# Optimization experiments

Hardware: AMD Instinct MI355X
Metric: run time of the kernel (lower is better)

The kernel has to match this reference:

```python
import jax, jax.numpy as jnp
import numpy as np

D = 1024        # number of Hawkes dimensions (N_g * K)
M = 32768       # number of events
BETA = 1.0      # fixed exponential-kernel decay
T_MAX = 1000    # observation horizon
EPS_MU = 1e-06
EPS_LOG = 1e-08


def setup_inputs() -> dict:
    key = jax.random.key(0)
    k1, k2, k3, k4 = jax.random.split(key, 4)
    t_events = jnp.sort(jax.random.uniform(k1, (M,), dtype=jnp.float32) * T_MAX)
    marks = jax.random.randint(k2, (M,), 0, D)
    # learned params around the torch init (-3 / -4) with a little noise
    log_mu = jnp.full((D,), -3.0, dtype=jnp.float32) + 0.1 * jax.random.normal(k3, (D,), dtype=jnp.float32)
    log_alpha = jnp.full((D, D), -4.0, dtype=jnp.float32) + 0.1 * jax.random.normal(k4, (D, D), dtype=jnp.float32)
    return {"t_events": t_events, "marks": marks, "log_mu": log_mu,
            "log_alpha": log_alpha, "T_max": T_MAX}


def reference(t_events, marks, log_mu, log_alpha, T_max):
    """Hawkes log-likelihood; faithful translation of XuHawkesTorch.intensity_loglik."""
    mu = jax.nn.softplus(log_mu) + EPS_MU          # [D]
    alpha = jax.nn.softplus(log_alpha)             # [D, D]
    T_max = jnp.asarray(T_max, dtype=t_events.dtype)

    # inter-event gaps; dt[0] = 0 so first event sees no decay (matches torch loop)
    dt = jnp.diff(t_events, prepend=t_events[:1])  # [M]
    decay = jnp.exp(-BETA * dt)                    # [M]

    def step(S, inp):
        dec, d = inp
        S = dec * S                                # exp-decay of excitation state
        lam_d = mu[d] + alpha[d] @ S               # intensity at event d
        ll = jnp.log(lam_d + EPS_LOG)
        S = S.at[d].add(1.0)                       # event adds unit excitation
        return S, ll

    S0 = jnp.zeros((D,), dtype=t_events.dtype)
    _, lls = jax.lax.scan(step, S0, (decay, marks))

    # compensator integral over [0, T_max]
    one_minus_exp = 1.0 - jnp.exp(-BETA * (T_max - t_events))   # [M]
    contrib = jax.ops.segment_sum(one_minus_exp, marks, num_segments=D)  # [D]
    integral = mu * T_max + alpha @ (contrib / BETA)            # [D]

    return lls.sum() - integral.sum()
```

## Files before the change

kernel.cpp:

```cpp
#include <hip/hip_runtime.h>


#define D 1024
#define M 32768
#define C 64
#define NC (M / C)
#define NB (NC * 4)
#define NG 16
#define GC (NC / NG)
#define TMAXV 1000.0f
#define EPSMU 1e-6f
#define EPSLOG 1e-8f

__device__ __forceinline__ float softplus(float x) {
    return (x > 0.0f) ? (x + log1pf(__expf(-x))) : log1pf(__expf(x));
}

__device__ __forceinline__ unsigned short f2bf(float x) {
    unsigned u = __float_as_uint(x);
    return (unsigned short)((u + 0x7FFFu + ((u >> 16) & 1u)) >> 16);
}
__device__ __forceinline__ float bf2f(unsigned short h) {
    return __uint_as_float(((unsigned)h) << 16);
}

__global__ void k_prep(const float* __restrict__ log_alpha, const float* __restrict__ log_mu,
                       unsigned short* __restrict__ ab, float* __restrict__ mu,
                       float* __restrict__ P) {
    int t = threadIdx.x;
    int b = blockIdx.x;
    if (b < 256) {
        int r0 = b * 4;
        float4 cs = {0.f, 0.f, 0.f, 0.f};
        for (int r = 0; r < 4; ++r) {
            const float4* src = (const float4*)(log_alpha + (size_t)(r0 + r) * D);
            float4 v = src[t];
            float4 a;
            a.x = softplus(v.x);
            a.y = softplus(v.y);
            a.z = softplus(v.z);
            a.w = softplus(v.w);
            cs.x += a.x; cs.y += a.y; cs.z += a.z; cs.w += a.w;
            ushort4 h;
            h.x = f2bf(a.x); h.y = f2bf(a.y); h.z = f2bf(a.z); h.w = f2bf(a.w);
            ((ushort4*)(ab + (size_t)(r0 + r) * D))[t] = h;
        }
        ((float4*)(P + (size_t)b * D))[t] = cs;
    } else {
#pragma unroll
        for (int q = 0; q < 4; ++q) {
            int k = t + 256 * q;
            mu[k] = softplus(log_mu[k]) + EPSMU;
        }
    }
}

__global__ void k_colred(const float* __restrict__ P, float* __restrict__ colsum) {
    __shared__ float red[8][32];
    int t = threadIdx.x;
    int colL = t & 31, seg = t >> 5;
    int col = blockIdx.x * 32 + colL;
    float s = 0.0f;
#pragma unroll 8
    for (int j = 0; j < 32; ++j)
        s += P[(size_t)(seg * 32 + j) * D + col];
    red[seg][colL] = s;
    __syncthreads();
    if (t < 32) {
        float v = 0.0f;
#pragma unroll
        for (int k = 0; k < 8; ++k) v += red[k][t];
        colsum[blockIdx.x * 32 + t] = v;
    }
}

__global__ void k_fused(const float* __restrict__ t_ev, const int* __restrict__ marks,
                        float* __restrict__ Sl, float* __restrict__ A) {
    __shared__ float Lh[GC * 256];
    __shared__ float dec[GC];
    __shared__ float tns[GC];
    int g = blockIdx.x >> 2, db = blockIdx.x & 3;
    int t = threadIdx.x;
#pragma unroll
    for (int q = 0; q < GC; ++q) Lh[q * 256 + t] = 0.0f;
    if (t < GC) {
        int gc = g * GC + t;
        float tn = (gc + 1 < NC) ? t_ev[(gc + 1) * C] : t_ev[M - 1];
        tns[t] = tn;
        dec[t] = (gc + 1 < NC) ? __expf(t_ev[gc * C] - tn) : 1.0f;
    }
    __syncthreads();
    int base = g * (GC * C);
#pragma unroll
    for (int it = 0; it < 8; ++it) {
        int e = it * 256 + t;
        float te = t_ev[base + e];
        int m = marks[base + e];
        int lc = e >> 6;
        int ml = m - db * 256;
        if ((unsigned)ml < 256u) atomicAdd(&Lh[lc * 256 + ml], __expf(te - tns[lc]));
    }
    __syncthreads();
    int k = db * 256 + t;
    float S = 0.0f;
    for (int lc = 0; lc < GC; ++lc) {
        Sl[(size_t)(g * GC + lc) * D + k] = S;
        S = S * dec[lc] + Lh[lc * 256 + t];
    }
    A[(size_t)g * D + k] = S;
}

__global__ void k_scanB(const float* __restrict__ t_ev, const float* __restrict__ A,
                        float* __restrict__ Sg, float* __restrict__ cumdec) {
    __shared__ float dec[NC];
    __shared__ float P[NG];
    int t = threadIdx.x;
    if (t < NC)
        dec[t] = (t + 1 < NC) ? __expf(t_ev[t * C] - t_ev[(t + 1) * C]) : 1.0f;
    __syncthreads();
    if (t < NC) {
        int g = t >> 5, r = t & 31;
        float p = 1.0f;
        for (int j = 0; j < r; ++j) p *= dec[g * GC + j];
        cumdec[t] = p;
        if (r == GC - 1) P[g] = p * dec[t];
    }
    __syncthreads();
    float a[NG];
#pragma unroll
    for (int g2 = 0; g2 < NG; ++g2) a[g2] = A[(size_t)g2 * D + t];
    float S = 0.0f;
#pragma unroll
    for (int g2 = 0; g2 < NG; ++g2) {
        Sg[(size_t)g2 * D + t] = S;
        S = S * P[g2] + a[g2];
    }
}

__launch_bounds__(256)
__global__ void k_main(const float* __restrict__ t_ev, const int* __restrict__ marks,
                       const unsigned short* __restrict__ ab, const float* __restrict__ mu,
                       const float* __restrict__ colsum, const float* __restrict__ Sl,
                       const float* __restrict__ Sg, const float* __restrict__ cumdec,
                       float* __restrict__ llp, float* __restrict__ compp) {
    __shared__ float S_lds[D];
    __shared__ float t_lds[C];
    __shared__ int d_lds[C];
    __shared__ float red[8];
    int t = threadIdx.x;
    int c = blockIdx.x >> 2, sub = blockIdx.x & 3;
    int g = c >> 5;
    float cd = cumdec[c];
#pragma unroll
    for (int q = 0; q < 4; ++q) {
        int k = t + 256 * q;
        S_lds[k] = Sl[(size_t)c * D + k] + Sg[(size_t)g * D + k] * cd;
    }
    if (t < C) {
        t_lds[t] = t_ev[c * C + t];
        d_lds[t] = marks[c * C + t];
    }
    __syncthreads();
    int wave = t >> 6, lane = t & 63;
    float t0 = t_lds[0];
    float ll_acc = 0.0f, comp_acc = 0.0f;
    for (int i = sub * 16 + wave; i < sub * 16 + 16; i += 4) {
        int row = d_lds[i];
        float ti = t_lds[i];
        float mu_r = mu[row];
        float cs_r = colsum[row];
        const uint4* arow = (const uint4*)(ab + (size_t)row * D);
        float acc_dot = 0.0f;
#pragma unroll
        for (int u = 0; u < 2; ++u) {
            uint4 pk = arow[2 * lane + u];
            const float4* sp = (const float4*)(S_lds + 16 * lane + 8 * u);
            float4 s0 = sp[0], s1 = sp[1];
            acc_dot += __uint_as_float(pk.x << 16) * s0.x
                     + __uint_as_float(pk.x & 0xFFFF0000u) * s0.y
                     + __uint_as_float(pk.y << 16) * s0.z
                     + __uint_as_float(pk.y & 0xFFFF0000u) * s0.w
                     + __uint_as_float(pk.z << 16) * s1.x
                     + __uint_as_float(pk.z & 0xFFFF0000u) * s1.y
                     + __uint_as_float(pk.w << 16) * s1.z
                     + __uint_as_float(pk.w & 0xFFFF0000u) * s1.w;
        }
        float part = acc_dot * __expf(t0 - ti);
        if (lane < i) {
            part += bf2f(ab[(size_t)row * D + d_lds[lane]]) * __expf(t_lds[lane] - ti);
        }
#pragma unroll
        for (int off = 32; off > 0; off >>= 1) part += __shfl_xor(part, off);
        if (lane == 0) {
            ll_acc += __logf(mu_r + part + EPSLOG);
            comp_acc += cs_r * (1.0f - __expf(ti - TMAXV));
        }
    }
    if (lane == 0) {
        red[wave] = ll_acc;
        red[4 + wave] = comp_acc;
    }
    __syncthreads();
    if (t == 0) {
        llp[blockIdx.x] = red[0] + red[1] + red[2] + red[3];
        compp[blockIdx.x] = red[4] + red[5] + red[6] + red[7];
    }
}

__global__ void k_final(const float* __restrict__ llp, const float* __restrict__ compp,
                        const float* __restrict__ mu, float* __restrict__ out) {
    __shared__ float r_ll[1024], r_cm[1024], r_mu[1024];
    int t = threadIdx.x;
    r_ll[t] = llp[t] + llp[t + 1024];
    r_cm[t] = compp[t] + compp[t + 1024];
    r_mu[t] = mu[t];
    __syncthreads();
    for (int off = 512; off > 0; off >>= 1) {
        if (t < off) {
            r_ll[t] += r_ll[t + off];
            r_cm[t] += r_cm[t + off];
            r_mu[t] += r_mu[t + off];
        }
        __syncthreads();
    }
    if (t == 0) out[0] = r_ll[0] - (TMAXV * r_mu[0] + r_cm[0]);
}

extern "C" void kernel_launch(void* const* d_in, const int* in_sizes, int n_in,
                              void* d_out, int out_size, void* d_ws, size_t ws_size,
                              hipStream_t stream) {
    const float* t_ev = (const float*)d_in[0];
    const int* marks = (const int*)d_in[1];
    const float* log_mu = (const float*)d_in[2];
    const float* log_alpha = (const float*)d_in[3];
    float* out = (float*)d_out;

    float* w = (float*)d_ws;
    unsigned short* ab = (unsigned short*)w;
    float* Sl = w + (size_t)D * D / 2;
    float* mu = Sl + (size_t)NC * D;
    float* colsum = mu + D;
    float* llp = colsum + D;
    float* compp = llp + NB;
    float* A = compp + NB;
    float* Sg = A + (size_t)NG * D;
    float* cumdec = Sg + (size_t)NG * D;
    float* P = Sl;

    k_prep<<<257, 256, 0, stream>>>(log_alpha, log_mu, ab, mu, P);
    k_colred<<<32, 256, 0, stream>>>(P, colsum);
    k_fused<<<64, 256, 0, stream>>>(t_ev, marks, Sl, A);
    k_scanB<<<1, 1024, 0, stream>>>(t_ev, A, Sg, cumdec);
    k_main<<<NB, 256, 0, stream>>>(t_ev, marks, ab, mu, colsum, Sl, Sg, cumdec, llp, compp);
    k_final<<<1, 1024, 0, stream>>>(llp, compp, mu, out);
}
```

Measured before the change: 98.54 us.

## Merge colsum reduction with block scan and split main kernel across more blocks

```diff
diff --git a/kernel.cpp b/kernel.cpp
--- a/kernel.cpp
+++ b/kernel.cpp
@@ -5,7 +5,7 @@
 #define M 32768
 #define C 64
 #define NC (M / C)
-#define NB (NC * 4)
+#define NB (NC * 8)
 #define NG 16
 #define GC (NC / NG)
 #define TMAXV 1000.0f
@@ -55,25 +55,6 @@
     }
 }
 
-__global__ void k_colred(const float* __restrict__ P, float* __restrict__ colsum) {
-    __shared__ float red[8][32];
-    int t = threadIdx.x;
-    int colL = t & 31, seg = t >> 5;
-    int col = blockIdx.x * 32 + colL;
-    float s = 0.0f;
-#pragma unroll 8
-    for (int j = 0; j < 32; ++j)
-        s += P[(size_t)(seg * 32 + j) * D + col];
-    red[seg][colL] = s;
-    __syncthreads();
-    if (t < 32) {
-        float v = 0.0f;
-#pragma unroll
-        for (int k = 0; k < 8; ++k) v += red[k][t];
-        colsum[blockIdx.x * 32 + t] = v;
-    }
-}
-
 __global__ void k_fused(const float* __restrict__ t_ev, const int* __restrict__ marks,
                         float* __restrict__ Sl, float* __restrict__ A) {
     __shared__ float Lh[GC * 256];
@@ -110,30 +91,49 @@
     A[(size_t)g * D + k] = S;
 }
 
-__global__ void k_scanB(const float* __restrict__ t_ev, const float* __restrict__ A,
-                        float* __restrict__ Sg, float* __restrict__ cumdec) {
-    __shared__ float dec[NC];
-    __shared__ float P[NG];
-    int t = threadIdx.x;
-    if (t < NC)
-        dec[t] = (t + 1 < NC) ? __expf(t_ev[t * C] - t_ev[(t + 1) * C]) : 1.0f;
-    __syncthreads();
-    if (t < NC) {
-        int g = t >> 5, r = t & 31;
-        float p = 1.0f;
-        for (int j = 0; j < r; ++j) p *= dec[g * GC + j];
-        cumdec[t] = p;
-        if (r == GC - 1) P[g] = p * dec[t];
-    }
-    __syncthreads();
-    float a[NG];
-#pragma unroll
-    for (int g2 = 0; g2 < NG; ++g2) a[g2] = A[(size_t)g2 * D + t];
-    float S = 0.0f;
-#pragma unroll
-    for (int g2 = 0; g2 < NG; ++g2) {
-        Sg[(size_t)g2 * D + t] = S;
-        S = S * P[g2] + a[g2];
+__global__ void k_mid(const float* __restrict__ P, float* __restrict__ colsum,
+                      const float* __restrict__ t_ev, const float* __restrict__ A,
+                      float* __restrict__ Sg, float* __restrict__ cumdec) {
+    int t = threadIdx.x;
+    if (blockIdx.x < 8) {
+        __shared__ float red[8][128];
+        int colL = t & 127, seg = t >> 7;
+        int col = blockIdx.x * 128 + colL;
+        float s = 0.0f;
+#pragma unroll
+        for (int j = 0; j < 32; ++j)
+            s += P[(size_t)(seg * 32 + j) * D + col];
+        red[seg][colL] = s;
+        __syncthreads();
+        if (t < 128) {
+            float v = 0.0f;
+#pragma unroll
+            for (int k = 0; k < 8; ++k) v += red[k][t];
+            colsum[blockIdx.x * 128 + t] = v;
+        }
+    } else {
+        __shared__ float dec[NC];
+        __shared__ float Pg[NG];
+        if (t < NC)
+            dec[t] = (t + 1 < NC) ? __expf(t_ev[t * C] - t_ev[(t + 1) * C]) : 1.0f;
+        __syncthreads();
+        if (t < NC) {
+            int g = t >> 5, r = t & 31;
+            float p = 1.0f;
+            for (int j = 0; j < r; ++j) p *= dec[g * GC + j];
+            cumdec[t] = p;
+            if (r == GC - 1) Pg[g] = p * dec[t];
+        }
+        __syncthreads();
+        float a[NG];
+#pragma unroll
+        for (int g2 = 0; g2 < NG; ++g2) a[g2] = A[(size_t)g2 * D + t];
+        float S = 0.0f;
+#pragma unroll
+        for (int g2 = 0; g2 < NG; ++g2) {
+            Sg[(size_t)g2 * D + t] = S;
+            S = S * Pg[g2] + a[g2];
+        }
     }
 }
 
@@ -148,7 +148,7 @@
     __shared__ int d_lds[C];
     __shared__ float red[8];
     int t = threadIdx.x;
-    int c = blockIdx.x >> 2, sub = blockIdx.x & 3;
+    int c = blockIdx.x >> 3, sub = blockIdx.x & 7;
     int g = c >> 5;
     float cd = cumdec[c];
 #pragma unroll
@@ -164,7 +164,8 @@
     int wave = t >> 6, lane = t & 63;
     float t0 = t_lds[0];
     float ll_acc = 0.0f, comp_acc = 0.0f;
-    for (int i = sub * 16 + wave; i < sub * 16 + 16; i += 4) {
+#pragma unroll
+    for (int i = sub * 8 + wave; i < sub * 8 + 8; i += 4) {
         int row = d_lds[i];
         float ti = t_lds[i];
         float mu_r = mu[row];
@@ -211,8 +212,14 @@
                         const float* __restrict__ mu, float* __restrict__ out) {
     __shared__ float r_ll[1024], r_cm[1024], r_mu[1024];
     int t = threadIdx.x;
-    r_ll[t] = llp[t] + llp[t + 1024];
-    r_cm[t] = compp[t] + compp[t + 1024];
+    float sll = 0.0f, scm = 0.0f;
+#pragma unroll
+    for (int j = 0; j < 4; ++j) {
+        sll += llp[t + 1024 * j];
+        scm += compp[t + 1024 * j];
+    }
+    r_ll[t] = sll;
+    r_cm[t] = scm;
     r_mu[t] = mu[t];
     __syncthreads();
     for (int off = 512; off > 0; off >>= 1) {
@@ -240,17 +247,16 @@
     float* Sl = w + (size_t)D * D / 2;
     float* mu = Sl + (size_t)NC * D;
     float* colsum = mu + D;
-    float* llp = colsum + D;
+    float* P = colsum + D;
+    float* llp = P + (size_t)256 * D;
     float* compp = llp + NB;
     float* A = compp + NB;
     float* Sg = A + (size_t)NG * D;
     float* cumdec = Sg + (size_t)NG * D;
-    float* P = Sl;
 
     k_prep<<<257, 256, 0, stream>>>(log_alpha, log_mu, ab, mu, P);
-    k_colred<<<32, 256, 0, stream>>>(P, colsum);
     k_fused<<<64, 256, 0, stream>>>(t_ev, marks, Sl, A);
-    k_scanB<<<1, 1024, 0, stream>>>(t_ev, A, Sg, cumdec);
+    k_mid<<<9, 1024, 0, stream>>>(P, colsum, t_ev, A, Sg, cumdec);
     k_main<<<NB, 256, 0, stream>>>(t_ev, marks, ab, mu, colsum, Sl, Sg, cumdec, llp, compp);
     k_final<<<1, 1024, 0, stream>>>(llp, compp, mu, out);
 }
```

Result: faster. 94.03 us (-4.6%).
